# Optimization experiments

Measured on AMD Instinct MI355X. Metric: run time of the kernel, lower is better.

The kernel has to match this reference:

```python
import jax, jax.numpy as jnp
import numpy as np

B, N, C, H = 2, 1024, 1024, 16
HD = C // H
SCALE = HD ** -0.5
TEMPERATURE = 0.8
TOP_K = 64
TOP_P = 0.9
NKAT_STRENGTH = 0.5
NKAT_DECAY = 0.95
LAYER_IDX = 2
NEG = jnp.float32(-1e9)  # stand-in for -inf; exp underflows to 0 after max-subtract


def setup_inputs() -> dict:
    key = jax.random.key(0)
    k0, k1, k2, k3 = jax.random.split(key, 4)
    x = jax.random.normal(k0, (B, N, C), dtype=jnp.float32)
    w_qkv = jax.random.normal(k1, (C, 3 * C), dtype=jnp.float32) * 0.02
    w_out = jax.random.normal(k2, (C, C), dtype=jnp.float32) * 0.02
    b_out = jnp.zeros((C,), dtype=jnp.float32)
    nkat_alpha = jnp.float32(0.1)
    nkat_beta = jnp.float32(0.05)
    return {"x": x, "w_qkv": w_qkv, "w_out": w_out, "b_out": b_out,
            "nkat_alpha": nkat_alpha, "nkat_beta": nkat_beta}


def _nkat_attention(x, w_qkv, w_out, b_out, nkat_alpha, nkat_beta):
    # qkv projection and head split
    qkv = (x @ w_qkv).reshape(B, N, 3, H, HD)
    q = jnp.transpose(qkv[:, :, 0], (0, 2, 1, 3))  # (B,H,N,HD)
    k = jnp.transpose(qkv[:, :, 1], (0, 2, 1, 3))
    v = jnp.transpose(qkv[:, :, 2], (0, 2, 1, 3))

    # scores + (zero) pos_bias + temperature scaling
    scores = jnp.einsum('bhqd,bhkd->bhqk', q, k) * SCALE
    scores = scores / max(TEMPERATURE, 1e-8)

    # top-k filtering: keep only the TOP_K largest scores per query
    kth = jax.lax.top_k(scores, TOP_K)[0][..., -1:]  # (B,H,N,1)
    scores = jnp.where(scores >= kth, scores, NEG)

    # nucleus (top-p) filtering: keep minimal prefix of sorted probs with
    # exclusive cumulative mass <= TOP_P (first element always kept)
    sorted_desc = -jnp.sort(-scores, axis=-1)
    probs = jax.nn.softmax(sorted_desc, axis=-1)
    cum = jnp.cumsum(probs, axis=-1)
    keep = (cum - probs) <= TOP_P  # exclusive cumsum <= p
    thr = jnp.min(jnp.where(keep, sorted_desc, jnp.inf), axis=-1, keepdims=True)
    scores = jnp.where(scores >= thr, scores, NEG)

    attn = jax.nn.softmax(scores, axis=-1)  # dropout p=0 -> identity (eval)

    # NKAT enhancement: per-token semantic modulation from x statistics
    layer_coeff = NKAT_STRENGTH * NKAT_DECAY ** LAYER_IDX
    token_mean = jnp.mean(x, axis=-1, keepdims=True)              # (B,N,1)
    token_var = jnp.mean((x - token_mean) ** 2, axis=-1, keepdims=True)
    theta = nkat_alpha * jnp.tanh(token_mean) + nkat_beta * jax.nn.sigmoid(token_var)
    attn = attn * (1.0 + layer_coeff * theta[:, None])            # (B,1,N,1) broadcast

    out = jnp.einsum('bhqk,bhkd->bhqd', attn, v)  # (B,H,N,HD)
    out = jnp.transpose(out, (0, 2, 1, 3)).reshape(B, N, C)
    return out @ w_out + b_out


def reference(x, w_qkv, w_out, b_out, nkat_alpha, nkat_beta):
    return _nkat_attention(x, w_qkv, w_out, b_out, nkat_alpha, nkat_beta)
```

## Files before the change

### kernel.cpp

```cpp
#include <hip/hip_runtime.h>

#define B_ 2
#define N_ 1024
#define C_ 1024
#define H_ 16
#define HD_ 64
#define KPAD 36
#define KPADL 40

typedef short short8 __attribute__((ext_vector_type(8)));
typedef float f32x4 __attribute__((ext_vector_type(4)));

union U16 {
  uint4 q;
  unsigned u[4];
  short8 s;
};

__device__ __forceinline__ float wsumf(float x) {
#pragma unroll
  for (int off = 32; off; off >>= 1) x += __shfl_xor(x, off, 64);
  return x;
}
__device__ __forceinline__ unsigned orderu(float f) {
  unsigned b = __float_as_uint(f);
  return (b & 0x80000000u) ? ~b : (b | 0x80000000u);
}
__device__ __forceinline__ float iorderu(unsigned x) {
  unsigned b = (x & 0x80000000u) ? (x & 0x7FFFFFFFu) : ~x;
  return __uint_as_float(b);
}

__device__ __forceinline__ unsigned splitf2(float f) {
  unsigned u = __float_as_uint(f);
  unsigned t = (u + 0x7fffu + ((u >> 16) & 1u)) & 0xffff0000u;
  float r = f - __uint_as_float(t);
  unsigned v = __float_as_uint(r);
  unsigned tv = v + 0x7fffu + ((v >> 16) & 1u);
  return (t >> 16) | (tv & 0xffff0000u);
}
__device__ __forceinline__ void splitf3(float f, unsigned& hm,
                                        unsigned short& lo) {
  unsigned u = __float_as_uint(f);
  unsigned t = (u + 0x7fffu + ((u >> 16) & 1u)) & 0xffff0000u;
  float r1 = f - __uint_as_float(t);
  unsigned v = __float_as_uint(r1);
  unsigned tv = (v + 0x7fffu + ((v >> 16) & 1u)) & 0xffff0000u;
  float r2 = r1 - __uint_as_float(tv);
  unsigned w = __float_as_uint(r2);
  unsigned tw = w + 0x7fffu + ((w >> 16) & 1u);
  hm = (t >> 16) | tv;
  lo = (unsigned short)(tw >> 16);
}

__device__ __forceinline__ void unpack_hm(const unsigned* p, short8& h,
                                          short8& l) {
  const uint4 X = *(const uint4*)p;
  const uint4 Y = *(const uint4*)(p + 4);
  U16 Hh, Ll;
  Hh.u[0] = (X.x & 0xffffu) | (X.y << 16);
  Hh.u[1] = (X.z & 0xffffu) | (X.w << 16);
  Hh.u[2] = (Y.x & 0xffffu) | (Y.y << 16);
  Hh.u[3] = (Y.z & 0xffffu) | (Y.w << 16);
  Ll.u[0] = (X.x >> 16) | (X.y & 0xffff0000u);
  Ll.u[1] = (X.z >> 16) | (X.w & 0xffff0000u);
  Ll.u[2] = (Y.x >> 16) | (Y.y & 0xffff0000u);
  Ll.u[3] = (Y.z >> 16) | (Y.w & 0xffff0000u);
  h = Hh.s;
  l = Ll.s;
}

__device__ __forceinline__ void mfma_core6(
    const float* __restrict__ A, const float* __restrict__ Bm, int lda,
    int ldb, int m0, int n0, unsigned* a_hm, unsigned* b_hm,
    unsigned short* a_lo, unsigned short* b_lo, f32x4 acc[4][2]) {
  const int tid = threadIdx.x;
  const int lane = tid & 63;
  const int wro = ((tid >> 7) & 1) * 64;
  const int wco = ((tid >> 6) & 1) * 32;
  const int a_k4 = (tid & 7) * 4, a_m = tid >> 3;
  const int b_k = tid >> 4;
  const int b_j4 = (tid & 15) * 4;
  const int fr = lane & 15, fk = (lane >> 4) * 8;

  float4 aR[4], bR[2];
#pragma unroll
  for (int j = 0; j < 4; ++j)
    aR[j] = *(const float4*)(A + (size_t)(m0 + a_m + 32 * j) * lda + a_k4);
  bR[0] = *(const float4*)(Bm + (size_t)b_k * ldb + n0 + b_j4);
  bR[1] = *(const float4*)(Bm + (size_t)(b_k + 16) * ldb + n0 + b_j4);

  for (int kt = 0; kt < 32; ++kt) {
    __syncthreads();
#pragma unroll
    for (int j = 0; j < 4; ++j) {
      uint4 w;
      ushort4 l;
      splitf3(aR[j].x, w.x, l.x);
      splitf3(aR[j].y, w.y, l.y);
      splitf3(aR[j].z, w.z, l.z);
      splitf3(aR[j].w, w.w, l.w);
      *(uint4*)(a_hm + (a_m + 32 * j) * KPAD + a_k4) = w;
      *(ushort4*)(a_lo + (a_m + 32 * j) * KPADL + a_k4) = l;
    }
    {
      unsigned hm;
      unsigned short lo;
      splitf3(bR[0].x, hm, lo);
      b_hm[(b_j4 + 0) * KPAD + b_k] = hm;
      b_lo[(b_j4 + 0) * KPADL + b_k] = lo;
      splitf3(bR[0].y, hm, lo);
      b_hm[(b_j4 + 1) * KPAD + b_k] = hm;
      b_lo[(b_j4 + 1) * KPADL + b_k] = lo;
      splitf3(bR[0].z, hm, lo);
      b_hm[(b_j4 + 2) * KPAD + b_k] = hm;
      b_lo[(b_j4 + 2) * KPADL + b_k] = lo;
      splitf3(bR[0].w, hm, lo);
      b_hm[(b_j4 + 3) * KPAD + b_k] = hm;
      b_lo[(b_j4 + 3) * KPADL + b_k] = lo;
      splitf3(bR[1].x, hm, lo);
      b_hm[(b_j4 + 0) * KPAD + b_k + 16] = hm;
      b_lo[(b_j4 + 0) * KPADL + b_k + 16] = lo;
      splitf3(bR[1].y, hm, lo);
      b_hm[(b_j4 + 1) * KPAD + b_k + 16] = hm;
      b_lo[(b_j4 + 1) * KPADL + b_k + 16] = lo;
      splitf3(bR[1].z, hm, lo);
      b_hm[(b_j4 + 2) * KPAD + b_k + 16] = hm;
      b_lo[(b_j4 + 2) * KPADL + b_k + 16] = lo;
      splitf3(bR[1].w, hm, lo);
      b_hm[(b_j4 + 3) * KPAD + b_k + 16] = hm;
      b_lo[(b_j4 + 3) * KPADL + b_k + 16] = lo;
    }
    __syncthreads();
    if (kt + 1 < 32) {
      const int kb = (kt + 1) * 32;
#pragma unroll
      for (int j = 0; j < 4; ++j)
        aR[j] =
            *(const float4*)(A + (size_t)(m0 + a_m + 32 * j) * lda + kb + a_k4);
      bR[0] = *(const float4*)(Bm + (size_t)(kb + b_k) * ldb + n0 + b_j4);
      bR[1] = *(const float4*)(Bm + (size_t)(kb + b_k + 16) * ldb + n0 + b_j4);
    }
    short8 ah[4], am[4], al[4];
#pragma unroll
    for (int rt = 0; rt < 4; ++rt) {
      const int row = wro + rt * 16 + fr;
      unpack_hm(a_hm + row * KPAD + fk, ah[rt], am[rt]);
      U16 L;
      L.q = *(const uint4*)(a_lo + row * KPADL + fk);
      al[rt] = L.s;
    }
#pragma unroll
    for (int ct = 0; ct < 2; ++ct) {
      const int row = wco + ct * 16 + fr;
      short8 bh, bm, bl;
      unpack_hm(b_hm + row * KPAD + fk, bh, bm);
      U16 L;
      L.q = *(const uint4*)(b_lo + row * KPADL + fk);
      bl = L.s;
#pragma unroll
      for (int rt = 0; rt < 4; ++rt) {
        f32x4 c = acc[rt][ct];
        c = __builtin_amdgcn_mfma_f32_16x16x32_bf16(ah[rt], bl, c, 0, 0, 0);
        c = __builtin_amdgcn_mfma_f32_16x16x32_bf16(al[rt], bh, c, 0, 0, 0);
        c = __builtin_amdgcn_mfma_f32_16x16x32_bf16(am[rt], bm, c, 0, 0, 0);
        c = __builtin_amdgcn_mfma_f32_16x16x32_bf16(ah[rt], bm, c, 0, 0, 0);
        c = __builtin_amdgcn_mfma_f32_16x16x32_bf16(am[rt], bh, c, 0, 0, 0);
        c = __builtin_amdgcn_mfma_f32_16x16x32_bf16(ah[rt], bh, c, 0, 0, 0);
        acc[rt][ct] = c;
      }
    }
  }
}

__device__ __forceinline__ void mfma_core3(const float* __restrict__ A,
                                           const float* __restrict__ Bm,
                                           int lda, int ldb, int m0, int n0,
                                           unsigned* a_hm, unsigned* b_hm,
                                           f32x4 acc[4][2]) {
  const int tid = threadIdx.x;
  const int lane = tid & 63;
  const int wro = ((tid >> 7) & 1) * 64;
  const int wco = ((tid >> 6) & 1) * 32;
  const int a_k4 = (tid & 7) * 4, a_m = tid >> 3;
  const int b_k = tid >> 4;
  const int b_j4 = (tid & 15) * 4;
  const int fr = lane & 15, fk = (lane >> 4) * 8;

  float4 aR[4], bR[2];
#pragma unroll
  for (int j = 0; j < 4; ++j)
    aR[j] = *(const float4*)(A + (size_t)(m0 + a_m + 32 * j) * lda + a_k4);
  bR[0] = *(const float4*)(Bm + (size_t)b_k * ldb + n0 + b_j4);
  bR[1] = *(const float4*)(Bm + (size_t)(b_k + 16) * ldb + n0 + b_j4);

  for (int kt = 0; kt < 32; ++kt) {
    __syncthreads();
#pragma unroll
    for (int j = 0; j < 4; ++j) {
      uint4 w;
      w.x = splitf2(aR[j].x);
      w.y = splitf2(aR[j].y);
      w.z = splitf2(aR[j].z);
      w.w = splitf2(aR[j].w);
      *(uint4*)(a_hm + (a_m + 32 * j) * KPAD + a_k4) = w;
    }
    {
      b_hm[(b_j4 + 0) * KPAD + b_k] = splitf2(bR[0].x);
      b_hm[(b_j4 + 1) * KPAD + b_k] = splitf2(bR[0].y);
      b_hm[(b_j4 + 2) * KPAD + b_k] = splitf2(bR[0].z);
      b_hm[(b_j4 + 3) * KPAD + b_k] = splitf2(bR[0].w);
      b_hm[(b_j4 + 0) * KPAD + b_k + 16] = splitf2(bR[1].x);
      b_hm[(b_j4 + 1) * KPAD + b_k + 16] = splitf2(bR[1].y);
      b_hm[(b_j4 + 2) * KPAD + b_k + 16] = splitf2(bR[1].z);
      b_hm[(b_j4 + 3) * KPAD + b_k + 16] = splitf2(bR[1].w);
    }
    __syncthreads();
    if (kt + 1 < 32) {
      const int kb = (kt + 1) * 32;
#pragma unroll
      for (int j = 0; j < 4; ++j)
        aR[j] =
            *(const float4*)(A + (size_t)(m0 + a_m + 32 * j) * lda + kb + a_k4);
      bR[0] = *(const float4*)(Bm + (size_t)(kb + b_k) * ldb + n0 + b_j4);
      bR[1] = *(const float4*)(Bm + (size_t)(kb + b_k + 16) * ldb + n0 + b_j4);
    }
    short8 ah[4], al[4];
#pragma unroll
    for (int rt = 0; rt < 4; ++rt)
      unpack_hm(a_hm + (wro + rt * 16 + fr) * KPAD + fk, ah[rt], al[rt]);
#pragma unroll
    for (int ct = 0; ct < 2; ++ct) {
      short8 bh, bl;
      unpack_hm(b_hm + (wco + ct * 16 + fr) * KPAD + fk, bh, bl);
#pragma unroll
      for (int rt = 0; rt < 4; ++rt) {
        f32x4 c = acc[rt][ct];
        c = __builtin_amdgcn_mfma_f32_16x16x32_bf16(ah[rt], bl, c, 0, 0, 0);
        c = __builtin_amdgcn_mfma_f32_16x16x32_bf16(al[rt], bh, c, 0, 0, 0);
        c = __builtin_amdgcn_mfma_f32_16x16x32_bf16(ah[rt], bh, c, 0, 0, 0);
        acc[rt][ct] = c;
      }
    }
  }
}

__global__ __launch_bounds__(256) void front_kernel(
    const float* __restrict__ x, const float* __restrict__ w,
    const float* __restrict__ alpha_p, const float* __restrict__ beta_p,
    float* __restrict__ q, float* __restrict__ ktb, float* __restrict__ v,
    float* __restrict__ fac) {
  __shared__ unsigned a_hm[128 * KPAD];
  __shared__ unsigned b_hm[64 * KPAD];
  __shared__ unsigned short a_lo[128 * KPADL];
  __shared__ unsigned short b_lo[64 * KPADL];

  const int bid = blockIdx.x;
  const int lane = threadIdx.x & 63;

  if (bid < 512) {
    f32x4 acc[4][2];
#pragma unroll
    for (int i = 0; i < 4; ++i)
#pragma unroll
      for (int j = 0; j < 2; ++j) acc[i][j] = (f32x4){0.f, 0.f, 0.f, 0.f};
    const int m0 = (bid >> 5) * 128, n0 = (bid & 31) * 64;
    mfma_core6(x, w, C_, 3 * C_, m0, n0, a_hm, b_hm, a_lo, b_lo, acc);

    const int wro = ((threadIdx.x >> 7) & 1) * 64;
    const int wco = ((threadIdx.x >> 6) & 1) * 32;
    const int rbase = (lane >> 4) * 4, cc = lane & 15;
#pragma unroll
    for (int rt = 0; rt < 4; ++rt) {
      const int m = m0 + wro + rt * 16 + rbase;
      const int bb2 = m >> 10, nn = m & 1023;
#pragma unroll
      for (int ct = 0; ct < 2; ++ct) {
        const int j = n0 + wco + ct * 16 + cc;
        const int sel = j >> 10, hh = (j >> 6) & 15, d0 = j & 63;
        const f32x4 c = acc[rt][ct];
        if (sel == 1) {
          *(float4*)(ktb + (((size_t)(bb2 * 16 + hh) * HD_ + d0) << 10) + nn) =
              make_float4(c[0], c[1], c[2], c[3]);
        } else {
          float* dst = q + (((size_t)(bb2 * 16 + hh) << 10) + nn) * HD_ + d0;
          dst[0] = c[0];
          dst[HD_] = c[1];
          dst[2 * HD_] = c[2];
          dst[3 * HD_] = c[3];
        }
      }
    }
  } else if (bid < 768) {
    f32x4 acc[4][2];
#pragma unroll
    for (int i = 0; i < 4; ++i)
#pragma unroll
      for (int j = 0; j < 2; ++j) acc[i][j] = (f32x4){0.f, 0.f, 0.f, 0.f};
    const int vb = bid - 512;
    const int m0 = (vb >> 4) * 128, n0 = 2048 + (vb & 15) * 64;
    mfma_core3(x, w, C_, 3 * C_, m0, n0, a_hm, b_hm, acc);

    const int wro = ((threadIdx.x >> 7) & 1) * 64;
    const int wco = ((threadIdx.x >> 6) & 1) * 32;
    const int rbase = (lane >> 4) * 4, cc = lane & 15;
#pragma unroll
    for (int rt = 0; rt < 4; ++rt) {
      const int m = m0 + wro + rt * 16 + rbase;
      const int bb = m >> 10, nn = m & 1023;
#pragma unroll
      for (int ct = 0; ct < 2; ++ct) {
        const int jv = (n0 - 2048) + wco + ct * 16 + cc;
        const int hh = (jv >> 6) & 15, d0 = jv & 63;
        const f32x4 c = acc[rt][ct];
        float* dst = v + (((size_t)(bb * 16 + hh) << 10) + nn) * HD_ + d0;
        dst[0] = c[0];
        dst[HD_] = c[1];
        dst[2 * HD_] = c[2];
        dst[3 * HD_] = c[3];
      }
    }
  } else {
    const int row = (bid - 768) * 4 + (threadIdx.x >> 6);
    const float4* xr = (const float4*)(x + (size_t)row * C_);
    float s = 0.f, ss = 0.f;
#pragma unroll
    for (int j = 0; j < 4; ++j) {
      float4 vv = xr[lane + 64 * j];
      s += vv.x + vv.y + vv.z + vv.w;
      ss += vv.x * vv.x + vv.y * vv.y + vv.z * vv.z + vv.w * vv.w;
    }
    s = wsumf(s);
    ss = wsumf(ss);
    const float mean = s * (1.f / 1024.f);
    const float var = ss * (1.f / 1024.f) - mean * mean;
    const float theta =
        alpha_p[0] * tanhf(mean) + beta_p[0] * (1.f / (1.f + __expf(-var)));
    if (lane == 0) fac[row] = 1.f + 0.45125f * theta;
  }
}

__global__ __launch_bounds__(256) void gemm_out_kernel(
    const float* __restrict__ a, const float* __restrict__ w,
    const float* __restrict__ bias, float* __restrict__ out) {
  __shared__ unsigned a_hm[128 * KPAD];
  __shared__ unsigned b_hm[64 * KPAD];
  f32x4 acc[4][2];
#pragma unroll
  for (int i = 0; i < 4; ++i)
#pragma unroll
    for (int j = 0; j < 2; ++j) acc[i][j] = (f32x4){0.f, 0.f, 0.f, 0.f};
  const int m0 = blockIdx.y * 128, n0 = blockIdx.x * 64;
  mfma_core3(a, w, C_, C_, m0, n0, a_hm, b_hm, acc);

  const int lane = threadIdx.x & 63;
  const int wro = ((threadIdx.x >> 7) & 1) * 64;
  const int wco = ((threadIdx.x >> 6) & 1) * 32;
  const int rbase = (lane >> 4) * 4, cc = lane & 15;
#pragma unroll
  for (int rt = 0; rt < 4; ++rt) {
    const int m = m0 + wro + rt * 16 + rbase;
#pragma unroll
    for (int ct = 0; ct < 2; ++ct) {
      const int j = n0 + wco + ct * 16 + cc;
      const float bj = bias[j];
      const f32x4 c = acc[rt][ct];
      float* dst = out + (size_t)m * C_ + j;
      dst[0] = c[0] + bj;
      dst[C_] = c[1] + bj;
      dst[2 * C_] = c[2] + bj;
      dst[3 * C_] = c[3] + bj;
    }
  }
}

__global__ __launch_bounds__(256) void attn_kernel(
    const float* __restrict__ qw, const float* __restrict__ kt,
    const float* __restrict__ vw, const float* __restrict__ fac,
    float* __restrict__ ao) {
  const int lane = threadIdx.x & 63;
  const int wid = threadIdx.x >> 6;
  const int qblk = blockIdx.x * 16;
  const int bh = qblk >> 10;
  const int b = bh >> 4, h = bh & 15;
  const int q0 = (qblk & (N_ - 1)) + wid * 4;

  __shared__ __align__(16) float q_ldsT[4][HD_][4];
  __shared__ unsigned su[4][64];
  __shared__ float sv[4][64];
  __shared__ int ck[4][64];
  __shared__ float cv[4][64];

  {
    const int qq = lane >> 4, dp = (lane & 15) << 2;
    const float4 v =
        *(const float4*)(qw + ((size_t)bh * N_ + q0 + qq) * HD_ + dp);
    q_ldsT[wid][dp + 0][qq] = v.x;
    q_ldsT[wid][dp + 1][qq] = v.y;
    q_ldsT[wid][dp + 2][qq] = v.z;
    q_ldsT[wid][dp + 3][qq] = v.w;
  }

  const float* ktb = kt + ((size_t)bh * HD_ * N_);
  const unsigned long long ltmask = (1ull << lane) - 1ull;
  unsigned u[4][16];

  for (int pass = 0; pass < 4; ++pass) {
    float acc[4][4];
#pragma unroll
    for (int a = 0; a < 4; ++a)
#pragma unroll
      for (int c = 0; c < 4; ++c) acc[a][c] = 0.f;
    const float* kp = ktb + (pass << 8) + (lane << 2);
#pragma unroll 4
    for (int d = 0; d < HD_; ++d) {
      const float4 kv = *(const float4*)(kp + (size_t)d * N_);
      const float4 qv = *(const float4*)(&q_ldsT[wid][d][0]);
      acc[0][0] = fmaf(kv.x, qv.x, acc[0][0]);
      acc[0][1] = fmaf(kv.x, qv.y, acc[0][1]);
      acc[0][2] = fmaf(kv.x, qv.z, acc[0][2]);
      acc[0][3] = fmaf(kv.x, qv.w, acc[0][3]);
      acc[1][0] = fmaf(kv.y, qv.x, acc[1][0]);
      acc[1][1] = fmaf(kv.y, qv.y, acc[1][1]);
      acc[1][2] = fmaf(kv.y, qv.z, acc[1][2]);
      acc[1][3] = fmaf(kv.y, qv.w, acc[1][3]);
      acc[2][0] = fmaf(kv.z, qv.x, acc[2][0]);
      acc[2][1] = fmaf(kv.z, qv.y, acc[2][1]);
      acc[2][2] = fmaf(kv.z, qv.z, acc[2][2]);
      acc[2][3] = fmaf(kv.z, qv.w, acc[2][3]);
      acc[3][0] = fmaf(kv.w, qv.x, acc[3][0]);
      acc[3][1] = fmaf(kv.w, qv.y, acc[3][1]);
      acc[3][2] = fmaf(kv.w, qv.z, acc[3][2]);
      acc[3][3] = fmaf(kv.w, qv.w, acc[3][3]);
    }
#pragma unroll
    for (int jl = 0; jl < 4; ++jl)
#pragma unroll
      for (int q = 0; q < 4; ++q)
        u[q][(pass << 2) + jl] = orderu((acc[jl][q] * 0.125f) / 0.8f);
  }

  unsigned mu[4], l0[4];
#pragma unroll
  for (int q = 0; q < 4; ++q) {
    unsigned mq = u[q][0];
#pragma unroll
    for (int j = 1; j < 16; ++j) mq = max(mq, u[q][j]);
    mu[q] = mq;
    l0[q] = mq;
  }
#pragma unroll
  for (int off = 32; off; off >>= 1) {
#pragma unroll
    for (int q = 0; q < 4; ++q) {
      mu[q] = max(mu[q], (unsigned)__shfl_xor((int)mu[q], off, 64));
      l0[q] = min(l0[q], (unsigned)__shfl_xor((int)l0[q], off, 64));
    }
  }

  unsigned lo[4], hi[4];
#pragma unroll
  for (int q = 0; q < 4; ++q) {
    lo[q] = l0[q];
    hi[q] = mu[q];
  }
  while ((lo[0] < hi[0]) | (lo[1] < hi[1]) | (lo[2] < hi[2]) |
         (lo[3] < hi[3])) {
#pragma unroll
    for (int q = 0; q < 4; ++q) {
      if (lo[q] < hi[q]) {
        const unsigned mid = lo[q] + ((hi[q] - lo[q]) >> 1) + 1u;
        int c = 0;
#pragma unroll
        for (int j = 0; j < 16; ++j)
          c += (int)__popcll(__ballot(u[q][j] >= mid));
        if (c >= 64) lo[q] = mid;
        else hi[q] = mid - 1u;
      }
    }
  }

  const float* vb = vw + ((size_t)bh << 16);
#pragma unroll
  for (int qq = 0; qq < 4; ++qq) {
    const unsigned kthu = lo[qq];
    const float m = iorderu(mu[qq]);

    float e[16];
    float zl = 0.f;
#pragma unroll
    for (int j = 0; j < 16; ++j) {
      const float ej = (u[qq][j] >= kthu) ? __expf(iorderu(u[qq][j]) - m) : 0.f;
      e[j] = ej;
      zl += ej;
    }
    const float Z = wsumf(zl);
    const float limit = 0.9f * Z;

    int base = 0;
#pragma unroll
    for (int j = 0; j < 16; ++j) {
      const bool f = (u[qq][j] >= kthu);
      const unsigned long long mb = __ballot(f);
      if (f) {
        const int pos = base + (int)__popcll(mb & ltmask);
        if (pos < 64) {
          su[wid][pos] = u[qq][j];
          sv[wid][pos] = e[j];
        }
      }
      base += (int)__popcll(mb);
    }

    unsigned sk = ~su[wid][lane];
    float se = sv[wid][lane];
#pragma unroll
    for (int k = 2; k <= 64; k <<= 1) {
#pragma unroll
      for (int j = k >> 1; j; j >>= 1) {
        const unsigned pk = (unsigned)__shfl_xor((int)sk, j, 64);
        const float pe = __shfl_xor(se, j, 64);
        const bool takeMin = (((lane & j) == 0) == ((lane & k) == 0));
        const bool sw = takeMin ? (pk < sk) : (pk > sk);
        if (sw) {
          sk = pk;
          se = pe;
        }
      }
    }

    float pre = se;
#pragma unroll
    for (int off = 1; off <= 32; off <<= 1) {
      const float t = __shfl_up(pre, off, 64);
      if (lane >= off) pre += t;
    }
    const float excl = pre - se;
    const bool keep = (excl <= limit);
    const unsigned long long km = __ballot(keep);
    const int L = 63 - __builtin_clzll(km);
    const unsigned thr = ~(unsigned)__shfl((int)sk, L, 64);

    float z2l = 0.f;
#pragma unroll
    for (int j = 0; j < 16; ++j) z2l += (u[qq][j] >= thr) ? e[j] : 0.f;
    const float Z2 = wsumf(z2l);
    const float wsc = fac[(b << 10) + q0 + qq] / Z2;

    int M = 0;
#pragma unroll
    for (int j = 0; j < 16; ++j) {
      const bool f = (u[qq][j] >= thr);
      const unsigned long long mb = __ballot(f);
      if (f) {
        const int pos = M + (int)__popcll(mb & ltmask);
        if (pos < 64) {
          ck[wid][pos] = ((j >> 2) << 8) + (lane << 2) + (j & 3);
          cv[wid][pos] = e[j] * wsc;
        }
      }
      M += (int)__popcll(mb);
    }
    if (M > 64) M = 64;

    float a0 = 0.f, a1 = 0.f, a2 = 0.f, a3 = 0.f;
    int i = 0;
    for (; i + 4 <= M; i += 4) {
      const int k0 = ck[wid][i], k1 = ck[wid][i + 1];
      const int k2 = ck[wid][i + 2], k3 = ck[wid][i + 3];
      const float c0 = cv[wid][i], c1 = cv[wid][i + 1];
      const float c2 = cv[wid][i + 2], c3 = cv[wid][i + 3];
      a0 = fmaf(c0, vb[((size_t)k0 << 6) + lane], a0);
      a1 = fmaf(c1, vb[((size_t)k1 << 6) + lane], a1);
      a2 = fmaf(c2, vb[((size_t)k2 << 6) + lane], a2);
      a3 = fmaf(c3, vb[((size_t)k3 << 6) + lane], a3);
    }
    for (; i < M; ++i)
      a0 = fmaf(cv[wid][i], vb[((size_t)ck[wid][i] << 6) + lane], a0);
    const float o = (a0 + a1) + (a2 + a3);

    ao[(((size_t)b << 10) + q0 + qq) * C_ + (h << 6) + lane] = o;
  }
}

extern "C" void kernel_launch(void* const* d_in, const int* in_sizes, int n_in,
                              void* d_out, int out_size, void* d_ws,
                              size_t ws_size, hipStream_t stream) {
  const float* x = (const float*)d_in[0];
  const float* wqkv = (const float*)d_in[1];
  const float* wout = (const float*)d_in[2];
  const float* bout = (const float*)d_in[3];
  const float* alpha = (const float*)d_in[4];
  const float* beta = (const float*)d_in[5];
  float* out = (float*)d_out;

  float* ws = (float*)d_ws;
  const size_t SZ = (size_t)B_ * H_ * N_ * HD_;
  float* qw = ws;
  float* kt = ws + SZ;
  float* vw = ws + 2 * SZ;
  float* ao = ws + 3 * SZ;
  float* fc = ws + 4 * SZ;

  front_kernel<<<1280, 256, 0, stream>>>(x, wqkv, alpha, beta, qw, kt, vw, fc);
  attn_kernel<<<(B_ * H_ * N_) / 16, 256, 0, stream>>>(qw, kt, vw, fc, ao);
  gemm_out_kernel<<<dim3(16, 16), 256, 0, stream>>>(ao, wout, bout, out);
}
```

Baseline: 376.9 us.

## Compute attention scores with bf16x3 MFMA using pre-split Q/K planes

```diff
diff --git a/kernel.cpp b/kernel.cpp
--- a/kernel.cpp
+++ b/kernel.cpp
@@ -10,6 +10,7 @@
 
 typedef short short8 __attribute__((ext_vector_type(8)));
 typedef float f32x4 __attribute__((ext_vector_type(4)));
+typedef unsigned short ushort_t;
 
 union U16 {
   uint4 q;
@@ -248,8 +249,10 @@
 __global__ __launch_bounds__(256) void front_kernel(
     const float* __restrict__ x, const float* __restrict__ w,
     const float* __restrict__ alpha_p, const float* __restrict__ beta_p,
-    float* __restrict__ q, float* __restrict__ ktb, float* __restrict__ v,
-    float* __restrict__ fac) {
+    ushort_t* __restrict__ qh, ushort_t* __restrict__ qm,
+    ushort_t* __restrict__ ql, ushort_t* __restrict__ kh,
+    ushort_t* __restrict__ km, ushort_t* __restrict__ kl,
+    float* __restrict__ v, float* __restrict__ fac) {
   __shared__ unsigned a_hm[128 * KPAD];
   __shared__ unsigned b_hm[64 * KPAD];
   __shared__ unsigned short a_lo[128 * KPADL];
@@ -279,15 +282,18 @@
         const int j = n0 + wco + ct * 16 + cc;
         const int sel = j >> 10, hh = (j >> 6) & 15, d0 = j & 63;
         const f32x4 c = acc[rt][ct];
-        if (sel == 1) {
-          *(float4*)(ktb + (((size_t)(bb2 * 16 + hh) * HD_ + d0) << 10) + nn) =
-              make_float4(c[0], c[1], c[2], c[3]);
-        } else {
-          float* dst = q + (((size_t)(bb2 * 16 + hh) << 10) + nn) * HD_ + d0;
-          dst[0] = c[0];
-          dst[HD_] = c[1];
-          dst[2 * HD_] = c[2];
-          dst[3 * HD_] = c[3];
+        ushort_t* ph = sel ? kh : qh;
+        ushort_t* pmid = sel ? km : qm;
+        ushort_t* plo = sel ? kl : ql;
+        const size_t bse = (((size_t)(bb2 * 16 + hh) << 10) + nn) * 64 + d0;
+#pragma unroll
+        for (int r = 0; r < 4; ++r) {
+          unsigned hmv;
+          unsigned short lov;
+          splitf3(c[r], hmv, lov);
+          ph[bse + 64 * r] = (ushort_t)(hmv & 0xffffu);
+          pmid[bse + 64 * r] = (ushort_t)(hmv >> 16);
+          plo[bse + 64 * r] = lov;
         }
       }
     }
@@ -375,7 +381,9 @@
 }
 
 __global__ __launch_bounds__(256) void attn_kernel(
-    const float* __restrict__ qw, const float* __restrict__ kt,
+    const ushort_t* __restrict__ qh, const ushort_t* __restrict__ qm,
+    const ushort_t* __restrict__ ql, const ushort_t* __restrict__ kh,
+    const ushort_t* __restrict__ km, const ushort_t* __restrict__ kl,
     const float* __restrict__ vw, const float* __restrict__ fac,
     float* __restrict__ ao) {
   const int lane = threadIdx.x & 63;
@@ -383,62 +391,66 @@
   const int qblk = blockIdx.x * 16;
   const int bh = qblk >> 10;
   const int b = bh >> 4, h = bh & 15;
-  const int q0 = (qblk & (N_ - 1)) + wid * 4;
-
-  __shared__ __align__(16) float q_ldsT[4][HD_][4];
-  __shared__ unsigned su[4][64];
-  __shared__ float sv[4][64];
-  __shared__ int ck[4][64];
-  __shared__ float cv[4][64];
-
-  {
-    const int qq = lane >> 4, dp = (lane & 15) << 2;
-    const float4 v =
-        *(const float4*)(qw + ((size_t)bh * N_ + q0 + qq) * HD_ + dp);
-    q_ldsT[wid][dp + 0][qq] = v.x;
-    q_ldsT[wid][dp + 1][qq] = v.y;
-    q_ldsT[wid][dp + 2][qq] = v.z;
-    q_ldsT[wid][dp + 3][qq] = v.w;
-  }
-
-  const float* ktb = kt + ((size_t)bh * HD_ * N_);
+  const int qbase = qblk & (N_ - 1);
+  const int q0 = qbase + wid * 4;
+
+  __shared__ unsigned S[16 * 1024];
+
+  const int fr = lane & 15, fko = (lane >> 4) * 8;
+
+  const size_t qoff = (((size_t)bh << 10) + qbase + fr) * 64 + fko;
+  short8 A[3][2];
+  A[0][0] = *(const short8*)(qh + qoff);
+  A[0][1] = *(const short8*)(qh + qoff + 32);
+  A[1][0] = *(const short8*)(qm + qoff);
+  A[1][1] = *(const short8*)(qm + qoff + 32);
+  A[2][0] = *(const short8*)(ql + qoff);
+  A[2][1] = *(const short8*)(ql + qoff + 32);
+
+  for (int t = 0; t < 16; ++t) {
+    const int key0 = (wid << 8) + (t << 4);
+    const size_t koff = (((size_t)bh << 10) + key0 + fr) * 64 + fko;
+    short8 Bf[3][2];
+    Bf[0][0] = *(const short8*)(kh + koff);
+    Bf[0][1] = *(const short8*)(kh + koff + 32);
+    Bf[1][0] = *(const short8*)(km + koff);
+    Bf[1][1] = *(const short8*)(km + koff + 32);
+    Bf[2][0] = *(const short8*)(kl + koff);
+    Bf[2][1] = *(const short8*)(kl + koff + 32);
+    f32x4 acc = (f32x4){0.f, 0.f, 0.f, 0.f};
+    acc = __builtin_amdgcn_mfma_f32_16x16x32_bf16(A[0][0], Bf[2][0], acc, 0, 0, 0);
+    acc = __builtin_amdgcn_mfma_f32_16x16x32_bf16(A[0][1], Bf[2][1], acc, 0, 0, 0);
+    acc = __builtin_amdgcn_mfma_f32_16x16x32_bf16(A[2][0], Bf[0][0], acc, 0, 0, 0);
+    acc = __builtin_amdgcn_mfma_f32_16x16x32_bf16(A[2][1], Bf[0][1], acc, 0, 0, 0);
+    acc = __builtin_amdgcn_mfma_f32_16x16x32_bf16(A[1][0], Bf[1][0], acc, 0, 0, 0);
+    acc = __builtin_amdgcn_mfma_f32_16x16x32_bf16(A[1][1], Bf[1][1], acc, 0, 0, 0);
+    acc = __builtin_amdgcn_mfma_f32_16x16x32_bf16(A[0][0], Bf[1][0], acc, 0, 0, 0);
+    acc = __builtin_amdgcn_mfma_f32_16x16x32_bf16(A[0][1], Bf[1][1], acc, 0, 0, 0);
+    acc = __builtin_amdgcn_mfma_f32_16x16x32_bf16(A[1][0], Bf[0][0], acc, 0, 0, 0);
+    acc = __builtin_amdgcn_mfma_f32_16x16x32_bf16(A[1][1], Bf[0][1], acc, 0, 0, 0);
+    acc = __builtin_amdgcn_mfma_f32_16x16x32_bf16(A[0][0], Bf[0][0], acc, 0, 0, 0);
+    acc = __builtin_amdgcn_mfma_f32_16x16x32_bf16(A[0][1], Bf[0][1], acc, 0, 0, 0);
+#pragma unroll
+    for (int r = 0; r < 4; ++r) {
+      const int qrow = (lane >> 4) * 4 + r;
+      S[(qrow << 10) + key0 + fr] = orderu((acc[r] * 0.125f) / 0.8f);
+    }
+  }
+  __syncthreads();
+
+  unsigned u[4][16];
+#pragma unroll
+  for (int qq = 0; qq < 4; ++qq)
+#pragma unroll
+    for (int j = 0; j < 16; ++j)
+      u[qq][j] = S[((wid * 4 + qq) << 10) + lane + (j << 6)];
+
+  unsigned* su_ = S + (wid << 12);
+  float* sv_ = (float*)(su_ + 64);
+  int* ck_ = (int*)(su_ + 128);
+  float* cv_ = (float*)(su_ + 192);
+
   const unsigned long long ltmask = (1ull << lane) - 1ull;
-  unsigned u[4][16];
-
-  for (int pass = 0; pass < 4; ++pass) {
-    float acc[4][4];
-#pragma unroll
-    for (int a = 0; a < 4; ++a)
-#pragma unroll
-      for (int c = 0; c < 4; ++c) acc[a][c] = 0.f;
-    const float* kp = ktb + (pass << 8) + (lane << 2);
-#pragma unroll 4
-    for (int d = 0; d < HD_; ++d) {
-      const float4 kv = *(const float4*)(kp + (size_t)d * N_);
-      const float4 qv = *(const float4*)(&q_ldsT[wid][d][0]);
-      acc[0][0] = fmaf(kv.x, qv.x, acc[0][0]);
-      acc[0][1] = fmaf(kv.x, qv.y, acc[0][1]);
-      acc[0][2] = fmaf(kv.x, qv.z, acc[0][2]);
-      acc[0][3] = fmaf(kv.x, qv.w, acc[0][3]);
-      acc[1][0] = fmaf(kv.y, qv.x, acc[1][0]);
-      acc[1][1] = fmaf(kv.y, qv.y, acc[1][1]);
-      acc[1][2] = fmaf(kv.y, qv.z, acc[1][2]);
-      acc[1][3] = fmaf(kv.y, qv.w, acc[1][3]);
-      acc[2][0] = fmaf(kv.z, qv.x, acc[2][0]);
-      acc[2][1] = fmaf(kv.z, qv.y, acc[2][1]);
-      acc[2][2] = fmaf(kv.z, qv.z, acc[2][2]);
-      acc[2][3] = fmaf(kv.z, qv.w, acc[2][3]);
-      acc[3][0] = fmaf(kv.w, qv.x, acc[3][0]);
-      acc[3][1] = fmaf(kv.w, qv.y, acc[3][1]);
-      acc[3][2] = fmaf(kv.w, qv.z, acc[3][2]);
-      acc[3][3] = fmaf(kv.w, qv.w, acc[3][3]);
-    }
-#pragma unroll
-    for (int jl = 0; jl < 4; ++jl)
-#pragma unroll
-      for (int q = 0; q < 4; ++q)
-        u[q][(pass << 2) + jl] = orderu((acc[jl][q] * 0.125f) / 0.8f);
-  }
 
   unsigned mu[4], l0[4];
 #pragma unroll
@@ -505,15 +517,15 @@
       if (f) {
         const int pos = base + (int)__popcll(mb & ltmask);
         if (pos < 64) {
-          su[wid][pos] = u[qq][j];
-          sv[wid][pos] = e[j];
+          su_[pos] = u[qq][j];
+          sv_[pos] = e[j];
         }
       }
       base += (int)__popcll(mb);
     }
 
-    unsigned sk = ~su[wid][lane];
-    float se = sv[wid][lane];
+    unsigned sk = ~su_[lane];
+    float se = sv_[lane];
 #pragma unroll
     for (int k = 2; k <= 64; k <<= 1) {
 #pragma unroll
@@ -537,8 +549,8 @@
     }
     const float excl = pre - se;
     const bool keep = (excl <= limit);
-    const unsigned long long km = __ballot(keep);
-    const int L = 63 - __builtin_clzll(km);
+    const unsigned long long km2 = __ballot(keep);
+    const int L = 63 - __builtin_clzll(km2);
     const unsigned thr = ~(unsigned)__shfl((int)sk, L, 64);
 
     float z2l = 0.f;
@@ -555,8 +567,8 @@
       if (f) {
         const int pos = M + (int)__popcll(mb & ltmask);
         if (pos < 64) {
-          ck[wid][pos] = ((j >> 2) << 8) + (lane << 2) + (j & 3);
-          cv[wid][pos] = e[j] * wsc;
+          ck_[pos] = lane + (j << 6);
+          cv_[pos] = e[j] * wsc;
         }
       }
       M += (int)__popcll(mb);
@@ -566,17 +578,17 @@
     float a0 = 0.f, a1 = 0.f, a2 = 0.f, a3 = 0.f;
     int i = 0;
     for (; i + 4 <= M; i += 4) {
-      const int k0 = ck[wid][i], k1 = ck[wid][i + 1];
-      const int k2 = ck[wid][i + 2], k3 = ck[wid][i + 3];
-      const float c0 = cv[wid][i], c1 = cv[wid][i + 1];
-      const float c2 = cv[wid][i + 2], c3 = cv[wid][i + 3];
+      const int k0 = ck_[i], k1 = ck_[i + 1];
+      const int k2 = ck_[i + 2], k3 = ck_[i + 3];
+      const float c0 = cv_[i], c1 = cv_[i + 1];
+      const float c2 = cv_[i + 2], c3 = cv_[i + 3];
       a0 = fmaf(c0, vb[((size_t)k0 << 6) + lane], a0);
       a1 = fmaf(c1, vb[((size_t)k1 << 6) + lane], a1);
       a2 = fmaf(c2, vb[((size_t)k2 << 6) + lane], a2);
       a3 = fmaf(c3, vb[((size_t)k3 << 6) + lane], a3);
     }
     for (; i < M; ++i)
-      a0 = fmaf(cv[wid][i], vb[((size_t)ck[wid][i] << 6) + lane], a0);
+      a0 = fmaf(cv_[i], vb[((size_t)ck_[i] << 6) + lane], a0);
     const float o = (a0 + a1) + (a2 + a3);
 
     ao[(((size_t)b << 10) + q0 + qq) * C_ + (h << 6) + lane] = o;
@@ -595,14 +607,21 @@
   float* out = (float*)d_out;
 
   float* ws = (float*)d_ws;
-  const size_t SZ = (size_t)B_ * H_ * N_ * HD_;
-  float* qw = ws;
-  float* kt = ws + SZ;
-  float* vw = ws + 2 * SZ;
-  float* ao = ws + 3 * SZ;
-  float* fc = ws + 4 * SZ;
-
-  front_kernel<<<1280, 256, 0, stream>>>(x, wqkv, alpha, beta, qw, kt, vw, fc);
-  attn_kernel<<<(B_ * H_ * N_) / 16, 256, 0, stream>>>(qw, kt, vw, fc, ao);
+  const size_t M1 = 1u << 20;
+  float* vw = ws;
+  float* ao = ws + 2 * M1;
+  float* fc = ws + 4 * M1;
+  ushort_t* pb = (ushort_t*)(ws + 4 * M1 + 4096);
+  ushort_t* qh = pb;
+  ushort_t* qm = pb + 2 * M1;
+  ushort_t* ql = pb + 4 * M1;
+  ushort_t* kh = pb + 6 * M1;
+  ushort_t* km = pb + 8 * M1;
+  ushort_t* kl = pb + 10 * M1;
+
+  front_kernel<<<1280, 256, 0, stream>>>(x, wqkv, alpha, beta, qh, qm, ql, kh,
+                                         km, kl, vw, fc);
+  attn_kernel<<<(B_ * H_ * N_) / 16, 256, 0, stream>>>(qh, qm, ql, kh, km, kl,
+                                                       vw, fc, ao);
   gemm_out_kernel<<<dim3(16, 16), 256, 0, stream>>>(ao, wout, bout, out);
 }
```

New measurement: 486.5 us. +29.1%, slower.
